# Kernel optimization log

Measured on AMD Instinct MI355X. Metric: run time of the kernel, lower is better.

## Reference

```python
import jax, jax.numpy as jnp
import numpy as np

B, T, V, E, H = 256, 64, 10000, 512, 1024

def setup_inputs() -> dict:
    key = jax.random.key(0)
    ks = jax.random.split(key, 8)
    seq = jax.random.randint(ks[0], (B, T), 0, V)
    seq_len = jax.random.randint(ks[1], (B, 1), 1, T + 1)
    seq_len = seq_len.at[0, 0].set(T)  # ensure max length == T (output time dim)
    std = 1.0 / np.sqrt(H)
    u = lambda k, s: jax.random.uniform(k, s, jnp.float32, -std, std)
    embed = jax.random.normal(ks[2], (V, E), jnp.float32) * 0.02
    x2h_w = u(ks[3], (E, 4 * H)); x2h_b = u(ks[4], (4 * H,))
    h2h_w = u(ks[5], (H, 4 * H)); h2h_b = u(ks[6], (4 * H,))
    aff_w = jax.random.uniform(ks[7], (H, H), jnp.float32, -std, std)
    aff_b = jnp.zeros((H,), jnp.float32)
    return {"seq": seq, "seq_len": seq_len, "embed": embed,
            "x2h_w": x2h_w, "x2h_b": x2h_b, "h2h_w": h2h_w, "h2h_b": h2h_b,
            "aff_w": aff_w, "aff_b": aff_b}


def reference(seq, seq_len, embed, x2h_w, x2h_b, h2h_w, h2h_b, aff_w, aff_b):
    b, t = seq.shape
    h_dim = h2h_w.shape[0]
    lens = seq_len[:, 0]                                   # [B]
    valid = jnp.arange(t)[None, :] < lens[:, None]         # [B,T] True where step is in-sequence
    x = embed[seq]                                         # [B,T,E]
    # Precompute input-to-hidden projection for all timesteps (one big GEMM).
    xg = jnp.einsum('bte,eg->btg', x, x2h_w) + x2h_b       # [B,T,4H]

    def step(carry, inp):
        h, c = carry
        xg_t, v_t = inp                                    # [B,4H], [B]
        gates = xg_t + h @ h2h_w + h2h_b
        i, f, g, o = jnp.split(gates, 4, axis=1)           # torch chunk order: in, forget, new_mem, out
        c_new = jax.nn.sigmoid(f) * c + jax.nn.sigmoid(i) * jnp.tanh(g)
        h_new = jax.nn.sigmoid(o) * jnp.tanh(c_new)
        v = v_t[:, None]
        # frozen state past each sequence's length (batch shrinks in torch loop)
        h2 = jnp.where(v, h_new, h)
        c2 = jnp.where(v, c_new, c)
        # recorded states are zero past the length (preallocated zeros in torch)
        return (h2, c2), (jnp.where(v, h_new, 0.0), jnp.where(v, c_new, 0.0))

    h0 = jnp.zeros((b, h_dim), xg.dtype)
    c0 = jnp.zeros((b, h_dim), xg.dtype)
    (h_last, _), (hs, cs) = jax.lax.scan(
        step, (h0, c0), (xg.transpose(1, 0, 2), valid.T))
    hidden_states = hs.transpose(1, 0, 2)                  # [B,T,H]
    memory_states = cs.transpose(1, 0, 2)                  # [B,T,H]
    final_hidden = jnp.tanh(h_last @ aff_w + aff_b)        # h at last valid step per sequence
    mask = valid.astype(jnp.float32)                       # == (memory_states.sum(2) != 0)
    return hidden_states, memory_states, final_hidden, mask
```

## Files before the change

kernel.cpp:

```cpp
#include <hip/hip_runtime.h>

#define B_ 256
#define T_ 64
#define V_ 10000
#define E_ 512
#define H_ 1024
#define G_ 4096
#define NWG_ 256

typedef __attribute__((ext_vector_type(8))) short short8;
typedef __attribute__((ext_vector_type(4))) float f32x4;

static __device__ __forceinline__ float bf2f(unsigned short u) {
    return __uint_as_float(((unsigned int)u) << 16);
}
static __device__ __forceinline__ unsigned short f2bf(float f) {
    unsigned int i = __float_as_uint(f);
    unsigned int r = (i + 0x7FFFu + ((i >> 16) & 1u)) >> 16;
    return (unsigned short)r;
}
static __device__ __forceinline__ float sigmoid_f(float x) {
    return 1.0f / (1.0f + __expf(-x));
}
static __device__ __forceinline__ float tanh_f(float x) {
    return 1.0f - 2.0f / (__expf(2.0f * x) + 1.0f);
}

static __device__ __forceinline__ void gload16(const void* g, void* l) {
    __builtin_amdgcn_global_load_lds((const __attribute__((address_space(1))) void*)g,
                                     (__attribute__((address_space(3))) void*)l, 16, 0, 0);
}

#define LD16C(dst, ptr) \
    asm volatile("global_load_dwordx4 %0, %1, off sc0 sc1" : "=v"(dst) : "v"(ptr))
#define DRAIN() do { asm volatile("s_waitcnt vmcnt(0)" ::: "memory"); \
                     __builtin_amdgcn_sched_barrier(0); } while (0)
#define STSHORTC(ptr, val) \
    asm volatile("global_store_short %0, %1, off sc0 sc1" :: "v"(ptr), "v"(val) : "memory")
#define STDWC(ptr, val) \
    asm volatile("global_store_dword %0, %1, off sc0 sc1" :: "v"(ptr), "v"(val) : "memory")

static __device__ __forceinline__ unsigned ld_u32_cohere(const void* p) {
    unsigned r;
    asm volatile("global_load_dword %0, %1, off sc0 sc1\n\ts_waitcnt vmcnt(0)"
                 : "=v"(r) : "v"(p) : "memory");
    return r;
}

__global__ __launch_bounds__(256) void k_cvt(const float* __restrict__ in,
                                             unsigned short* __restrict__ out, int n4) {
    int i = blockIdx.x * 256 + threadIdx.x;
    if (i >= n4) return;
    float4 v = reinterpret_cast<const float4*>(in)[i];
    uint2 p;
    p.x = (unsigned int)f2bf(v.x) | ((unsigned int)f2bf(v.y) << 16);
    p.y = (unsigned int)f2bf(v.z) | ((unsigned int)f2bf(v.w) << 16);
    reinterpret_cast<uint2*>(out)[i] = p;
}

__global__ __launch_bounds__(256) void k_transpose(const float* __restrict__ w,
                                                   unsigned short* __restrict__ wT,
                                                   int K, int N) {
    __shared__ float tile[32][33];
    int nblk = N >> 5;
    int bx = blockIdx.x % nblk;
    int by = blockIdx.x / nblk;
    int lx = threadIdx.x & 31;
    int ly = threadIdx.x >> 5;
    int k0 = by * 32, n0 = bx * 32;
#pragma unroll
    for (int i = 0; i < 32; i += 8)
        tile[ly + i][lx] = w[(size_t)(k0 + ly + i) * N + n0 + lx];
    __syncthreads();
#pragma unroll
    for (int i = 0; i < 32; i += 8)
        wT[(size_t)(n0 + ly + i) * K + k0 + lx] = f2bf(tile[lx][ly + i]);
}

__global__ __launch_bounds__(256) void k_xg(const int* __restrict__ seq,
                                            const unsigned short* __restrict__ emb,
                                            const unsigned short* __restrict__ wT,
                                            const float* __restrict__ bias,
                                            unsigned short* __restrict__ xg) {
    const int mt = blockIdx.x & 127;
    const int nt = blockIdx.x >> 7;
    const int tid = threadIdx.x;
    const int w = tid >> 6, l = tid & 63, g = l >> 4, li = l & 15;
    const int wr = w >> 1, wc = w & 1;

    __shared__ unsigned short As[128 * 32];
    __shared__ unsigned short Bs[128 * 32];
    __shared__ int seqv[128];

    if (tid < 128) seqv[tid] = seq[mt * 128 + tid];
    __syncthreads();

    const int r0 = w * 16 + (l >> 2);
    const int kc = (l & 3) * 8;
    const unsigned short* asrc0 = emb + (size_t)seqv[r0] * E_ + kc;
    const unsigned short* asrc1 = emb + (size_t)seqv[r0 + 64] * E_ + kc;
    const unsigned short* bsrc0 = wT + (size_t)(nt * 128 + r0) * E_ + kc;
    const unsigned short* bsrc1 = wT + (size_t)(nt * 128 + r0 + 64) * E_ + kc;
    char* aldsw = (char*)As + w * 1024;
    char* bldsw = (char*)Bs + w * 1024;

    f32x4 acc[4][4] = {};
    for (int k0 = 0; k0 < E_; k0 += 32) {
        gload16(asrc0 + k0, aldsw);
        gload16(asrc1 + k0, aldsw + 4096);
        gload16(bsrc0 + k0, bldsw);
        gload16(bsrc1 + k0, bldsw + 4096);
        __syncthreads();
        short8 af[4], bf[4];
#pragma unroll
        for (int i = 0; i < 4; ++i) {
            af[i] = *(const short8*)(As + (wr * 64 + i * 16 + li) * 32 + g * 8);
            bf[i] = *(const short8*)(Bs + (wc * 64 + i * 16 + li) * 32 + g * 8);
        }
#pragma unroll
        for (int i = 0; i < 4; ++i)
#pragma unroll
            for (int j = 0; j < 4; ++j)
                acc[i][j] = __builtin_amdgcn_mfma_f32_16x16x32_bf16(af[i], bf[j], acc[i][j], 0, 0, 0);
        __syncthreads();
    }

#pragma unroll
    for (int j = 0; j < 4; ++j) {
        const int col = nt * 128 + wc * 64 + j * 16 + li;
        const float bv = bias[col];
#pragma unroll
        for (int i = 0; i < 4; ++i) {
            const int row = mt * 128 + wr * 64 + i * 16 + g * 4;
#pragma unroll
            for (int r = 0; r < 4; ++r)
                xg[(size_t)(row + r) * G_ + col] = f2bf(acc[i][j][r] + bv);
        }
    }
}

__global__ __launch_bounds__(256) void k_rnn(const unsigned short* __restrict__ xg,
                                             const unsigned short* __restrict__ wT,
                                             const float* __restrict__ bias,
                                             const int* __restrict__ seq_len,
                                             unsigned short* __restrict__ h0,
                                             unsigned short* __restrict__ h1,
                                             float* __restrict__ hs,
                                             float* __restrict__ cs,
                                             unsigned int* __restrict__ flags) {
    const int wg = blockIdx.x;
    const int rb = wg >> 6, cb = wg & 63;
    const int tid = threadIdx.x;
    const int w = tid >> 6, l = tid & 63, g = l >> 4, li = l & 15;

    __shared__ unsigned short Bs[64 * 1024];

    for (int gi = 0; gi < 32; ++gi) {
        int gidx = gi * 256 + tid;
        int ls = gidx & 63;
        int kks = (gidx >> 6) & 31;
        int qs = gidx >> 11;
        int col = qs * 1024 + cb * 16 + (ls & 15);
        int ko = kks * 32 + (ls >> 4) * 8;
        int4 v = *(const int4*)(wT + (size_t)col * H_ + ko);
        *(int4*)((char*)Bs + (size_t)gidx * 16) = v;
    }

    const int hc = cb * 16 + li;
    float bv[4];
#pragma unroll
    for (int q = 0; q < 4; ++q) bv[q] = bias[q * 1024 + hc];
    const int m0 = rb * 64 + w * 16 + g * 4;
    int sl[4];
#pragma unroll
    for (int r = 0; r < 4; ++r) sl[r] = seq_len[m0 + r];
    float creg[4] = {0.f, 0.f, 0.f, 0.f};
    float hreg[4] = {0.f, 0.f, 0.f, 0.f};

    const int arow_i = rb * 64 + w * 16 + li;
    const char* bbase = (const char*)Bs + l * 16;
    const unsigned int* fp = flags + (rb << 6) + tid;

    __syncthreads();

#define LOADS(buf, c) do { _Pragma("unroll") \
    for (int p = 0; p < 8; ++p) LD16C(buf[p], arowc + ((c) + p) * 64); } while (0)

#define MFMAS(buf, c) do { _Pragma("unroll") \
    for (int p = 0; p < 8; ++p) { \
        const int kk = (c) + p; \
        _Pragma("unroll") \
        for (int q = 0; q < 4; ++q) { \
            short8 bfv = *(const short8*)(bbase + ((q * 32 + kk) << 10)); \
            acc[q] = __builtin_amdgcn_mfma_f32_16x16x32_bf16(buf[p], bfv, acc[q], 0, 0, 0); \
        } } } while (0)

    unsigned short xgr[4][4];
#pragma unroll
    for (int r = 0; r < 4; ++r) {
        const size_t xoff = ((size_t)(m0 + r) * T_ + 0) * G_ + hc;
#pragma unroll
        for (int q = 0; q < 4; ++q) xgr[r][q] = xg[xoff + q * 1024];
    }
    asm volatile("" ::: "memory");

    for (int t = 0; t < T_; ++t) {
        const unsigned short* h_in = (t & 1) ? h1 : h0;
        unsigned short* h_out = (t & 1) ? h0 : h1;
        const char* arowc = (const char*)(h_in + (size_t)arow_i * H_ + g * 8);

        f32x4 acc[4] = {};
        short8 A0[8], A1[8];
        LOADS(A0, 0);
        DRAIN();
        LOADS(A1, 8);
        MFMAS(A0, 0);
        DRAIN();
        LOADS(A0, 16);
        MFMAS(A1, 8);
        DRAIN();
        LOADS(A1, 24);
        MFMAS(A0, 16);
        DRAIN();
        MFMAS(A1, 24);

        float hsv[4], csv[4];
#pragma unroll
        for (int r = 0; r < 4; ++r) {
            const int m = m0 + r;
            float ig = sigmoid_f(acc[0][r] + bv[0] + bf2f(xgr[r][0]));
            float fg = sigmoid_f(acc[1][r] + bv[1] + bf2f(xgr[r][1]));
            float gg = tanh_f(acc[2][r] + bv[2] + bf2f(xgr[r][2]));
            float og = sigmoid_f(acc[3][r] + bv[3] + bf2f(xgr[r][3]));
            float cn = fg * creg[r] + ig * gg;
            float hn = og * tanh_f(cn);
            bool valid = t < sl[r];
            if (valid) { creg[r] = cn; hreg[r] = hn; }
            hsv[r] = valid ? hn : 0.0f;
            csv[r] = valid ? cn : 0.0f;
            STSHORTC(h_out + (size_t)m * H_ + hc, f2bf(hreg[r]));
        }

        DRAIN();
        __syncthreads();
        const unsigned int tp1 = (unsigned int)(t + 1);
        if (tid == 0) {
            STDWC(flags + wg, tp1);
        }

#pragma unroll
        for (int r = 0; r < 4; ++r) {
            const size_t ooff = ((size_t)(m0 + r) * T_ + t) * H_ + hc;
            __builtin_nontemporal_store(hsv[r], &hs[ooff]);
            __builtin_nontemporal_store(csv[r], &cs[ooff]);
        }

        if (t < T_ - 1) {
#pragma unroll
            for (int r = 0; r < 4; ++r) {
                const size_t xoff = ((size_t)(m0 + r) * T_ + (t + 1)) * G_ + hc;
#pragma unroll
                for (int q = 0; q < 4; ++q) xgr[r][q] = xg[xoff + q * 1024];
            }
            asm volatile("" ::: "memory");
            if (tid < 64) {
                while (ld_u32_cohere(fp) < tp1) __builtin_amdgcn_s_sleep(1);
            }
            __syncthreads();
        }
    }
#undef LOADS
#undef MFMAS
}

__global__ __launch_bounds__(256) void k_final(const unsigned short* __restrict__ h,
                                               const unsigned short* __restrict__ wT,
                                               const float* __restrict__ bias,
                                               float* __restrict__ fin) {
    const int rb = blockIdx.x & 3;
    const int nb = blockIdx.x >> 2;
    const int tid = threadIdx.x;
    const int w = tid >> 6;
    const int l = tid & 63;
    const int g = l >> 4, li = l & 15;

    __shared__ unsigned short As[64][40];
    __shared__ unsigned short Bs[64][40];

    const int srow = tid >> 2;
    const int scol = (tid & 3) * 8;
    const unsigned short* aptr = h + (size_t)(rb * 64 + srow) * H_ + scol;
    const unsigned short* bptr = wT + (size_t)(nb * 64 + srow) * H_ + scol;

    f32x4 acc[4] = {};
    int4 ra = *(const int4*)aptr;
    int4 rb2 = *(const int4*)bptr;
    for (int kk = 0; kk < H_; kk += 32) {
        *(int4*)&As[srow][scol] = ra;
        *(int4*)&Bs[srow][scol] = rb2;
        __syncthreads();
        if (kk + 32 < H_) {
            ra = *(const int4*)(aptr + kk + 32);
            rb2 = *(const int4*)(bptr + kk + 32);
        }
        short8 af = *(const short8*)&As[w * 16 + li][g * 8];
#pragma unroll
        for (int q = 0; q < 4; ++q) {
            short8 bf = *(const short8*)&Bs[q * 16 + li][g * 8];
            acc[q] = __builtin_amdgcn_mfma_f32_16x16x32_bf16(af, bf, acc[q], 0, 0, 0);
        }
        __syncthreads();
    }
    const int m0 = rb * 64 + w * 16 + g * 4;
#pragma unroll
    for (int q = 0; q < 4; ++q) {
        int col = nb * 64 + q * 16 + li;
        float bv = bias[col];
#pragma unroll
        for (int r = 0; r < 4; ++r)
            fin[(size_t)(m0 + r) * H_ + col] = tanh_f(acc[q][r] + bv);
    }
}

__global__ __launch_bounds__(256) void k_mask(const int* __restrict__ seq_len,
                                              float* __restrict__ mask) {
    int i = blockIdx.x * 256 + threadIdx.x;
    int b = i >> 6, t = i & 63;
    mask[i] = (t < seq_len[b]) ? 1.0f : 0.0f;
}

extern "C" void kernel_launch(void* const* d_in, const int* in_sizes, int n_in,
                              void* d_out, int out_size, void* d_ws, size_t ws_size,
                              hipStream_t stream) {
    const int* seq = (const int*)d_in[0];
    const int* seq_len = (const int*)d_in[1];
    const float* embed = (const float*)d_in[2];
    const float* x2h_w = (const float*)d_in[3];
    const float* x2h_b = (const float*)d_in[4];
    const float* h2h_w = (const float*)d_in[5];
    const float* h2h_b = (const float*)d_in[6];
    const float* aff_w = (const float*)d_in[7];
    const float* aff_b = (const float*)d_in[8];

    float* out = (float*)d_out;
    float* hs = out;
    float* cs = out + (size_t)B_ * T_ * H_;
    float* fin = cs + (size_t)B_ * T_ * H_;
    float* mask = fin + (size_t)B_ * H_;

    char* p = (char*)d_ws;
    unsigned short* emb_b = (unsigned short*)p; p += (size_t)V_ * E_ * 2;
    unsigned short* x2h_t = (unsigned short*)p; p += (size_t)G_ * E_ * 2;
    unsigned short* h2h_t = (unsigned short*)p; p += (size_t)G_ * H_ * 2;
    unsigned short* aff_t = (unsigned short*)p; p += (size_t)H_ * H_ * 2;
    unsigned short* xg    = (unsigned short*)p; p += (size_t)B_ * T_ * G_ * 2;
    unsigned short* hbuf0 = (unsigned short*)p; p += (size_t)B_ * H_ * 2;
    unsigned short* hbuf1 = (unsigned short*)p; p += (size_t)B_ * H_ * 2;
    unsigned int*   flags = (unsigned int*)p;   p += NWG_ * sizeof(unsigned int);

    hipLaunchKernelGGL(k_cvt, dim3((V_ * E_ / 4 + 255) / 256), dim3(256), 0, stream,
                       embed, emb_b, V_ * E_ / 4);
    hipLaunchKernelGGL(k_transpose, dim3((E_ / 32) * (G_ / 32)), dim3(256), 0, stream,
                       x2h_w, x2h_t, E_, G_);
    hipLaunchKernelGGL(k_transpose, dim3((H_ / 32) * (G_ / 32)), dim3(256), 0, stream,
                       h2h_w, h2h_t, H_, G_);
    hipLaunchKernelGGL(k_transpose, dim3((H_ / 32) * (H_ / 32)), dim3(256), 0, stream,
                       aff_w, aff_t, H_, H_);

    hipLaunchKernelGGL(k_xg, dim3(128 * 32), dim3(256), 0, stream,
                       seq, emb_b, x2h_t, x2h_b, xg);

    hipMemsetAsync(hbuf0, 0, (size_t)B_ * H_ * 2, stream);
    hipMemsetAsync(flags, 0, NWG_ * sizeof(unsigned int), stream);

    {
        const unsigned short* xg_p = xg;
        const unsigned short* wT_p = h2h_t;
        const float* b_p = h2h_b;
        const int* sl_p = seq_len;
        unsigned short* h0_p = hbuf0;
        unsigned short* h1_p = hbuf1;
        float* hs_p = hs;
        float* cs_p = cs;
        unsigned int* fl_p = flags;
        void* args[] = {(void*)&xg_p, (void*)&wT_p, (void*)&b_p, (void*)&sl_p,
                        (void*)&h0_p, (void*)&h1_p, (void*)&hs_p, (void*)&cs_p,
                        (void*)&fl_p};
        hipLaunchCooperativeKernel(reinterpret_cast<void*>(k_rnn), dim3(NWG_), dim3(256),
                                   args, 0, stream);
    }

    hipLaunchKernelGGL(k_final, dim3(64), dim3(256), 0, stream, hbuf0, aff_t, aff_b, fin);
    hipLaunchKernelGGL(k_mask, dim3(B_ * T_ / 256), dim3(256), 0, stream, seq_len, mask);
}
```

Before: 674.8 us.

## Interleave row-block mapping, load full h row upfront, use acquire fence

Changes the workgroup-to-tile mapping so the four row blocks are interleaved (rb = wg&3) and the per-step flag layout changes to match. It replaces the double-buffered cache-bypassing inline-asm loads with plain loads of all 32 A fragments before the MFMA loop, and adds an agent-scope acquire atomic load after the barrier so the plain loads observe other workgroups' h writes. The aim is to cut the manual drain stalls and let the compiler schedule loads, at the cost of more registers and a reliance on acquire semantics for cross-workgroup coherence.

```diff
diff --git a/kernel.cpp b/kernel.cpp
--- a/kernel.cpp
+++ b/kernel.cpp
@@ -31,8 +31,6 @@
                                      (__attribute__((address_space(3))) void*)l, 16, 0, 0);
 }
 
-#define LD16C(dst, ptr) \
-    asm volatile("global_load_dwordx4 %0, %1, off sc0 sc1" : "=v"(dst) : "v"(ptr))
 #define DRAIN() do { asm volatile("s_waitcnt vmcnt(0)" ::: "memory"); \
                      __builtin_amdgcn_sched_barrier(0); } while (0)
 #define STSHORTC(ptr, val) \
@@ -149,7 +147,7 @@
                                              float* __restrict__ cs,
                                              unsigned int* __restrict__ flags) {
     const int wg = blockIdx.x;
-    const int rb = wg >> 6, cb = wg & 63;
+    const int rb = wg & 3, cb = wg >> 2;
     const int tid = threadIdx.x;
     const int w = tid >> 6, l = tid & 63, g = l >> 4, li = l & 15;
 
@@ -179,21 +177,9 @@
 
     const int arow_i = rb * 64 + w * 16 + li;
     const char* bbase = (const char*)Bs + l * 16;
-    const unsigned int* fp = flags + (rb << 6) + tid;
+    const unsigned int* fp = flags + rb + 4 * tid;
 
     __syncthreads();
-
-#define LOADS(buf, c) do { _Pragma("unroll") \
-    for (int p = 0; p < 8; ++p) LD16C(buf[p], arowc + ((c) + p) * 64); } while (0)
-
-#define MFMAS(buf, c) do { _Pragma("unroll") \
-    for (int p = 0; p < 8; ++p) { \
-        const int kk = (c) + p; \
-        _Pragma("unroll") \
-        for (int q = 0; q < 4; ++q) { \
-            short8 bfv = *(const short8*)(bbase + ((q * 32 + kk) << 10)); \
-            acc[q] = __builtin_amdgcn_mfma_f32_16x16x32_bf16(buf[p], bfv, acc[q], 0, 0, 0); \
-        } } } while (0)
 
     unsigned short xgr[4][4];
 #pragma unroll
@@ -202,27 +188,25 @@
 #pragma unroll
         for (int q = 0; q < 4; ++q) xgr[r][q] = xg[xoff + q * 1024];
     }
-    asm volatile("" ::: "memory");
 
     for (int t = 0; t < T_; ++t) {
         const unsigned short* h_in = (t & 1) ? h1 : h0;
         unsigned short* h_out = (t & 1) ? h0 : h1;
-        const char* arowc = (const char*)(h_in + (size_t)arow_i * H_ + g * 8);
+        const char* arowc = (const char*)(h_in + (size_t)arow_i * H_) + g * 16;
+
+        short8 A[32];
+#pragma unroll
+        for (int p = 0; p < 32; ++p) A[p] = *(const short8*)(arowc + p * 64);
 
         f32x4 acc[4] = {};
-        short8 A0[8], A1[8];
-        LOADS(A0, 0);
-        DRAIN();
-        LOADS(A1, 8);
-        MFMAS(A0, 0);
-        DRAIN();
-        LOADS(A0, 16);
-        MFMAS(A1, 8);
-        DRAIN();
-        LOADS(A1, 24);
-        MFMAS(A0, 16);
-        DRAIN();
-        MFMAS(A1, 24);
+#pragma unroll
+        for (int kk = 0; kk < 32; ++kk) {
+#pragma unroll
+            for (int q = 0; q < 4; ++q) {
+                short8 bfv = *(const short8*)(bbase + ((q * 32 + kk) << 10));
+                acc[q] = __builtin_amdgcn_mfma_f32_16x16x32_bf16(A[kk], bfv, acc[q], 0, 0, 0);
+            }
+        }
 
         float hsv[4], csv[4];
 #pragma unroll
@@ -267,10 +251,11 @@
                 while (ld_u32_cohere(fp) < tp1) __builtin_amdgcn_s_sleep(1);
             }
             __syncthreads();
-        }
-    }
-#undef LOADS
-#undef MFMAS
+            unsigned av = __hip_atomic_load(flags + wg, __ATOMIC_ACQUIRE,
+                                            __HIP_MEMORY_SCOPE_AGENT);
+            asm volatile("" :: "v"(av));
+        }
+    }
 }
 
 __global__ __launch_bounds__(256) void k_final(const unsigned short* __restrict__ h,
```

After: 1.111 ms. +64.6%, slower.
